# Kernel optimization log

Hardware: AMD Instinct MI355X
Metric: run time of the kernel (lower is better)

## Reference

```python
import jax, jax.numpy as jnp
import numpy as np

NUM_HEADS = 12
LN_EPS = 1e-12


def setup_inputs() -> dict:
    key = jax.random.key(0)
    ks = jax.random.split(key, 18)
    B, S, H, I, P, KW = 8, 128, 768, 3072, 50, 100
    s = 0.02
    inp = {
        'hidden_state': jax.random.normal(ks[0], (B, S, H), jnp.float32),
        'positive_keywords': jax.random.normal(ks[1], (P, H), jnp.float32),
        'negative_keywords': jax.random.normal(ks[2], (P, H), jnp.float32),
        'attention_mask': jnp.zeros((B, 1, 1, S), jnp.float32),
        # Bilinear weights: out = (x @ W) * keyword
        'Wq': jax.random.normal(ks[3], (H, H), jnp.float32) * s,
        'Wk': jax.random.normal(ks[4], (H, H), jnp.float32) * s,
        'Wv': jax.random.normal(ks[5], (H, H), jnp.float32) * s,
        'Wo': jax.random.normal(ks[6], (H, H), jnp.float32) * s,
        'bo': jnp.zeros((H,), jnp.float32),
        # mlp: Linear(kwcount, 1)
        'Wmlp': jax.random.normal(ks[7], (KW,), jnp.float32) * s,
        'bmlp': jnp.zeros((), jnp.float32),
        # Bottleneck FFN
        'Wdown': jax.random.normal(ks[8], (H, I), jnp.float32) * s,
        'bdown': jnp.zeros((I,), jnp.float32),
        'Wup': jax.random.normal(ks[9], (I, H), jnp.float32) * s,
        'bup': jnp.zeros((H,), jnp.float32),
        'gamma': jnp.ones((H,), jnp.float32),
        'beta': jnp.zeros((H,), jnp.float32),
    }
    return inp


def reference(hidden_state, positive_keywords, negative_keywords, attention_mask,
              Wq, Wk, Wv, Wo, bo, Wmlp, bmlp, Wdown, bdown, Wup, bup, gamma, beta):
    B, S, H = hidden_state.shape
    nh = NUM_HEADS
    hd = H // nh
    # interleave pos/neg keywords -> pool [KW, H] (diff == 0, no padding)
    pool = jnp.stack((positive_keywords, negative_keywords), axis=1).reshape(-1, H)

    # shared sequence projections (keyword modulates elementwise afterwards)
    PQ = hidden_state @ Wq  # [B,S,H]
    PK = hidden_state @ Wk
    PV = hidden_state @ Wv
    scale = 1.0 / jnp.sqrt(jnp.float32(hd))

    def per_kw(kw):  # kw: [H]
        def heads(P):
            return (P * kw).reshape(B, S, nh, hd).transpose(0, 2, 1, 3)  # [B,nh,S,hd]
        Q, K, V = heads(PQ), heads(PK), heads(PV)
        scores = jnp.einsum('bhqd,bhkd->bhqk', Q, K) * scale + attention_mask
        # NOTE: softmax over dim=-2 (query axis), faithful to the original
        w = jax.nn.softmax(scores, axis=-2)
        ctx = jnp.einsum('bhqk,bhkd->bhqd', w, V)
        ctx = ctx.transpose(0, 2, 1, 3).reshape(B, S, H)
        return ctx @ Wo + bo  # [B,S,H]

    stacked = jax.vmap(per_kw)(pool)  # [KW,B,S,H]
    # mlp Linear(KW,1) over the stacked keyword axis
    fused = jnp.einsum('kbsh,k->bsh', stacked, Wmlp) + bmlp  # [B,S,H]

    # Bottleneck FFN + residual LayerNorm (dropout = identity in eval)
    down = jax.nn.gelu(fused @ Wdown + bdown, approximate=False)
    up = down @ Wup + bup
    x = up + fused
    mu = jnp.mean(x, axis=-1, keepdims=True)
    var = jnp.var(x, axis=-1, keepdims=True)
    return gamma * (x - mu) / jnp.sqrt(var + LN_EPS) + beta
```

## Files before the change

kernel.cpp:

```cpp
#include <hip/hip_runtime.h>
#include <hip/hip_bf16.h>
#include <math.h>

#define B_ 8
#define S_ 128
#define H_ 768
#define NH_ 12
#define HD_ 64
#define M_ 1024
#define KW_ 100
#define I_ 3072
#define QKVN 2304
#define NCHUNK 5
#define KWPER 20
#define LOG2E 1.4426950408889634f

typedef __attribute__((ext_vector_type(8))) short short8;
typedef __attribute__((ext_vector_type(8))) unsigned short ushort8;
typedef __attribute__((ext_vector_type(4))) float f32x4;
typedef __attribute__((ext_vector_type(4))) short s4b;

static __device__ __forceinline__ unsigned short f2b(float f) {
  union { float f; unsigned int u; } v; v.f = f;
  return (unsigned short)((v.u + 0x7fffu + ((v.u >> 16) & 1u)) >> 16);
}
static __device__ __forceinline__ float b2f(unsigned short b) {
  union { unsigned int u; float f; } v; v.u = ((unsigned int)b) << 16;
  return v.f;
}
static __device__ __forceinline__ void gload16(const unsigned short* g, unsigned short* l) {
  __builtin_amdgcn_global_load_lds((const __attribute__((address_space(1))) unsigned int*)g,
                                   (__attribute__((address_space(3))) unsigned int*)l, 16, 0, 0);
}

__global__ void k_prep(const float* __restrict__ hidden,
                       const float* __restrict__ Wq, const float* __restrict__ Wk,
                       const float* __restrict__ Wv, const float* __restrict__ Wo,
                       const float* __restrict__ Wdown, const float* __restrict__ Wup,
                       const float* __restrict__ posk, const float* __restrict__ negk,
                       const float* __restrict__ Wmlp, const float* __restrict__ bmlp,
                       const float* __restrict__ bo,
                       unsigned short* __restrict__ hb, unsigned short* __restrict__ qkvT,
                       unsigned short* __restrict__ WoT, unsigned short* __restrict__ WdownT,
                       unsigned short* __restrict__ WupT,
                       float* __restrict__ kw2s, float* __restrict__ kwm, float* __restrict__ c0) {
  __shared__ float tile[32][33];
  int z = blockIdx.z;
  int t = threadIdx.x;
  if (z == 6) {
    int n = blockIdx.y * 96 + blockIdx.x;
    if (n < 768) {
      int i = (n * 256 + t) * 4;
      float4 v = *(const float4*)&hidden[i];
      uint2 o;
      o.x = (unsigned)f2b(v.x) | ((unsigned)f2b(v.y) << 16);
      o.y = (unsigned)f2b(v.z) | ((unsigned)f2b(v.w) << 16);
      *(uint2*)&hb[i] = o;
    } else if (n < 1068) {
      int idx = (n - 768) * 256 + t;
      if (idx < KW_ * H_) {
        int j = idx / H_, d = idx - j * H_;
        float v = (j & 1) ? negk[(j >> 1) * H_ + d] : posk[(j >> 1) * H_ + d];
        kw2s[idx] = v * v * 0.125f * LOG2E;
        kwm[idx] = v * Wmlp[j];
      }
    } else if (n == 1068) {
      __shared__ float red[256];
      red[t] = (t < KW_) ? Wmlp[t] : 0.f;
      __syncthreads();
      for (int s = 128; s > 0; s >>= 1) { if (t < s) red[t] += red[t + s]; __syncthreads(); }
      float sWm = red[0];
      for (int c = t; c < H_; c += 256) c0[c] = sWm * bo[c] + bmlp[0];
    }
    return;
  }
  const float* src; unsigned short* dst; int R, C, r0, c0t;
  if (z < 4) {
    if (blockIdx.x >= 24) return;
    const float* srcs[4] = {Wq, Wk, Wv, Wo};
    src = srcs[z];
    dst = (z < 3) ? qkvT + (size_t)z * 768 * 768 : WoT;
    R = 768; C = 768; c0t = blockIdx.x * 32; r0 = blockIdx.y * 32;
  } else if (z == 4) {
    src = Wdown; dst = WdownT; R = 768; C = 3072;
    c0t = blockIdx.x * 32; r0 = blockIdx.y * 32;
  } else {
    src = Wup; dst = WupT; R = 3072; C = 768;
    c0t = blockIdx.y * 32; r0 = blockIdx.x * 32;
  }
  int tx = t & 31, ty = t >> 5;
#pragma unroll
  for (int i = 0; i < 4; i++)
    tile[ty + i * 8][tx] = src[(size_t)(r0 + ty + i * 8) * C + c0t + tx];
  __syncthreads();
#pragma unroll
  for (int i = 0; i < 4; i++)
    dst[(size_t)(c0t + ty + i * 8) * R + r0 + tx] = f2b(tile[tx][ty + i * 8]);
}

template <int EPI>
__launch_bounds__(256)
__global__ void k_gemm_bt(const unsigned short* __restrict__ A, const unsigned short* __restrict__ BT,
                          int M, int N, int K,
                          float* __restrict__ outF, unsigned short* __restrict__ outB,
                          const float* __restrict__ bias, const float* __restrict__ res) {
  __shared__ __align__(16) unsigned short Asm[128 * 32];
  __shared__ __align__(16) unsigned short Bsm[128 * 32];
  int tid = threadIdx.x;
  int lane = tid & 63, wid = tid >> 6;
  int g = lane >> 4, c16 = lane & 15;
  int wr = wid >> 1, wc = wid & 1;
  int m0 = blockIdx.y * 128, n0 = blockIdx.x * 128;
  f32x4 acc[4][4] = {};
  int ldsrow = lane >> 2, ldscol = (lane & 3) * 8;
  for (int kt = 0; kt < K; kt += 32) {
    __syncthreads();
#pragma unroll
    for (int r = 0; r < 2; r++) {
      int c = wid * 2 + r;
      gload16(A + (size_t)(m0 + c * 16 + ldsrow) * K + kt + ldscol, &Asm[c * 512 + lane * 8]);
      gload16(BT + (size_t)(n0 + c * 16 + ldsrow) * K + kt + ldscol, &Bsm[c * 512 + lane * 8]);
    }
    __syncthreads();
    short8 af[4], bf[4];
#pragma unroll
    for (int mi = 0; mi < 4; mi++) af[mi] = *(const short8*)&Asm[(wr * 64 + mi * 16 + c16) * 32 + g * 8];
#pragma unroll
    for (int ni = 0; ni < 4; ni++) bf[ni] = *(const short8*)&Bsm[(wc * 64 + ni * 16 + c16) * 32 + g * 8];
#pragma unroll
    for (int mi = 0; mi < 4; mi++)
#pragma unroll
      for (int ni = 0; ni < 4; ni++)
        acc[mi][ni] = __builtin_amdgcn_mfma_f32_16x16x32_bf16(af[mi], bf[ni], acc[mi][ni], 0, 0, 0);
  }
#pragma unroll
  for (int mi = 0; mi < 4; mi++)
#pragma unroll
    for (int ni = 0; ni < 4; ni++)
#pragma unroll
      for (int rr = 0; rr < 4; rr++) {
        int row = m0 + wr * 64 + mi * 16 + g * 4 + rr;
        int col = n0 + wc * 64 + ni * 16 + c16;
        float v = acc[mi][ni][rr];
        if (EPI == 0) {
          outB[(size_t)row * N + col] = f2b(v);
        } else if (EPI == 2) {
          float t = v + bias[col];
          float gl = 0.5f * t * (1.f + erff(t * 0.70710678118f));
          outB[(size_t)row * N + col] = f2b(gl);
        }
      }
}

template <int OUTB>
__launch_bounds__(256)
__global__ void k_gemm_sk(const unsigned short* __restrict__ A, const unsigned short* __restrict__ BT,
                          int M, int N, int K, int ksl, void* __restrict__ pOut) {
  __shared__ __align__(16) unsigned short Asm[128 * 32];
  __shared__ __align__(16) unsigned short Bsm[128 * 32];
  int tid = threadIdx.x;
  int lane = tid & 63, wid = tid >> 6;
  int g = lane >> 4, c16 = lane & 15;
  int wr = wid >> 1, wc = wid & 1;
  int m0 = blockIdx.y * 128, n0 = blockIdx.x * 128;
  int kstart = blockIdx.z * ksl;
  f32x4 acc[4][4] = {};
  int ldsrow = lane >> 2, ldscol = (lane & 3) * 8;
  for (int kt = 0; kt < ksl; kt += 32) {
    __syncthreads();
#pragma unroll
    for (int r = 0; r < 2; r++) {
      int c = wid * 2 + r;
      gload16(A + (size_t)(m0 + c * 16 + ldsrow) * K + kstart + kt + ldscol, &Asm[c * 512 + lane * 8]);
      gload16(BT + (size_t)(n0 + c * 16 + ldsrow) * K + kstart + kt + ldscol, &Bsm[c * 512 + lane * 8]);
    }
    __syncthreads();
    short8 af[4], bf[4];
#pragma unroll
    for (int mi = 0; mi < 4; mi++) af[mi] = *(const short8*)&Asm[(wr * 64 + mi * 16 + c16) * 32 + g * 8];
#pragma unroll
    for (int ni = 0; ni < 4; ni++) bf[ni] = *(const short8*)&Bsm[(wc * 64 + ni * 16 + c16) * 32 + g * 8];
#pragma unroll
    for (int mi = 0; mi < 4; mi++)
#pragma unroll
      for (int ni = 0; ni < 4; ni++)
        acc[mi][ni] = __builtin_amdgcn_mfma_f32_16x16x32_bf16(af[mi], bf[ni], acc[mi][ni], 0, 0, 0);
  }
#pragma unroll
  for (int mi = 0; mi < 4; mi++)
#pragma unroll
    for (int ni = 0; ni < 4; ni++)
#pragma unroll
      for (int rr = 0; rr < 4; rr++) {
        int row = m0 + wr * 64 + mi * 16 + g * 4 + rr;
        int col = n0 + wc * 64 + ni * 16 + c16;
        if (OUTB) {
          unsigned short* dst = (unsigned short*)pOut + (size_t)blockIdx.z * M * N;
          dst[(size_t)row * N + col] = f2b(acc[mi][ni][rr]);
        } else {
          float* dst = (float*)pOut + (size_t)blockIdx.z * M * N;
          dst[(size_t)row * N + col] = acc[mi][ni][rr];
        }
      }
}

template <int SPLITS, int EPI>
__global__ void k_red(const float* __restrict__ p, const float* __restrict__ bias,
                      float* __restrict__ outF, unsigned short* __restrict__ outB, int N) {
  int i = (blockIdx.x * 256 + threadIdx.x) * 4;
  const size_t MN = (size_t)M_ * N;
  float4 s = *(const float4*)&p[i];
#pragma unroll
  for (int c = 1; c < SPLITS; c++) {
    float4 v = *(const float4*)&p[c * MN + i];
    s.x += v.x; s.y += v.y; s.z += v.z; s.w += v.w;
  }
  if (EPI == 1) {
    int col = i % N;
    s.x += bias[col]; s.y += bias[col + 1]; s.z += bias[col + 2]; s.w += bias[col + 3];
    *(float4*)&outF[i] = s;
  }
  uint2 o;
  o.x = (unsigned)f2b(s.x) | ((unsigned)f2b(s.y) << 16);
  o.y = (unsigned)f2b(s.z) | ((unsigned)f2b(s.w) << 16);
  *(uint2*)&outB[i] = o;
}

template <int SPLITS>
__global__ void k_redb(const unsigned short* __restrict__ p, unsigned short* __restrict__ outB,
                       size_t MN) {
  int i = (blockIdx.x * 256 + threadIdx.x) * 4;
  float s0 = 0.f, s1 = 0.f, s2 = 0.f, s3 = 0.f;
#pragma unroll
  for (int c = 0; c < SPLITS; c++) {
    uint2 v = *(const uint2*)&p[c * MN + i];
    s0 += b2f((unsigned short)(v.x & 0xffffu));
    s1 += b2f((unsigned short)(v.x >> 16));
    s2 += b2f((unsigned short)(v.y & 0xffffu));
    s3 += b2f((unsigned short)(v.y >> 16));
  }
  uint2 o;
  o.x = (unsigned)f2b(s0) | ((unsigned)f2b(s1) << 16);
  o.y = (unsigned)f2b(s2) | ((unsigned)f2b(s3) << 16);
  *(uint2*)&outB[i] = o;
}

__launch_bounds__(512, 2)
__global__ void k_attn(const unsigned short* __restrict__ PQKV,
                       const float* __restrict__ kw2s, const float* __restrict__ kwm,
                       unsigned short* __restrict__ partial) {
  __shared__ __align__(16) char SM[67584];
  int tid = threadIdx.x;
  int lane = tid & 63, wid = tid >> 6;
  int g = (lane >> 4) & 3, c16 = lane & 15;
  int n = blockIdx.x;
  int chunk = (n >> 3) % NCHUNK;
  int hb = (n & 7) + 8 * (n / (8 * NCHUNK));
  int h = hb >> 3, b = hb & 7;
  const size_t rowbase = (size_t)b * 128 * QKVN;
  const unsigned short* Qbase = PQKV + rowbase + h * HD_;
  const unsigned short* Kbase = Qbase + H_;
  const unsigned short* Vbase = Qbase + 2 * H_;

  unsigned short (*QS)[72] = (unsigned short(*)[72])SM;
  unsigned short (*VS)[72] = (unsigned short(*)[72])(SM + 18432);
  {
    int kq = tid >> 2, quarter = tid & 3;
    const unsigned short* srcq = Qbase + (size_t)kq * QKVN + quarter * 16;
    ushort8 a0 = *(const ushort8*)srcq;
    ushort8 a1 = *(const ushort8*)(srcq + 8);
    *(ushort8*)&QS[kq][quarter * 16] = a0;
    *(ushort8*)&QS[kq][quarter * 16 + 8] = a1;
    const unsigned short* srcv = Vbase + (size_t)kq * QKVN + quarter * 16;
    ushort8 w0 = *(const ushort8*)srcv;
    ushort8 w1 = *(const ushort8*)(srcv + 8);
    *(ushort8*)&VS[kq][quarter * 16] = w0;
    *(ushort8*)&VS[kq][quarter * 16 + 8] = w1;
  }
  const unsigned short* kpg = Kbase + (size_t)(wid * 16 + c16) * QKVN;
  ushort8 kraw0 = *(const ushort8*)(kpg + g * 8);
  ushort8 kraw1 = *(const ushort8*)(kpg + 32 + g * 8);
  __syncthreads();
  unsigned short vraw[4][4];
#pragma unroll
  for (int dt = 0; dt < 4; dt++)
#pragma unroll
    for (int j = 0; j < 4; j++)
      vraw[dt][j] = VS[wid * 16 + 4 * g + j][dt * 16 + c16];

  f32x4 acc[4][8] = {};
  int zo = 0;
  asm volatile("" : "+v"(zo));
  for (int ki = 0; ki < KWPER; ki++) {
    int kwi = chunk * KWPER + ki;
    const float* k2p = kw2s + (size_t)kwi * H_ + h * HD_;
    const float* kmp = kwm + (size_t)kwi * H_ + h * HD_;
    short8 kA0, kA1;
    {
      float4 s0 = *(const float4*)(k2p + g * 8);
      float4 s1 = *(const float4*)(k2p + g * 8 + 4);
      float4 s2 = *(const float4*)(k2p + 32 + g * 8);
      float4 s3 = *(const float4*)(k2p + 32 + g * 8 + 4);
      union { unsigned u[4]; short8 v; } p0, p1;
      asm("v_cvt_pk_bf16_f32 %0, %1, %2" : "=v"(p0.u[0]) : "v"(b2f(kraw0[0]) * s0.x), "v"(b2f(kraw0[1]) * s0.y));
      asm("v_cvt_pk_bf16_f32 %0, %1, %2" : "=v"(p0.u[1]) : "v"(b2f(kraw0[2]) * s0.z), "v"(b2f(kraw0[3]) * s0.w));
      asm("v_cvt_pk_bf16_f32 %0, %1, %2" : "=v"(p0.u[2]) : "v"(b2f(kraw0[4]) * s1.x), "v"(b2f(kraw0[5]) * s1.y));
      asm("v_cvt_pk_bf16_f32 %0, %1, %2" : "=v"(p0.u[3]) : "v"(b2f(kraw0[6]) * s1.z), "v"(b2f(kraw0[7]) * s1.w));
      asm("v_cvt_pk_bf16_f32 %0, %1, %2" : "=v"(p1.u[0]) : "v"(b2f(kraw1[0]) * s2.x), "v"(b2f(kraw1[1]) * s2.y));
      asm("v_cvt_pk_bf16_f32 %0, %1, %2" : "=v"(p1.u[1]) : "v"(b2f(kraw1[2]) * s2.z), "v"(b2f(kraw1[3]) * s2.w));
      asm("v_cvt_pk_bf16_f32 %0, %1, %2" : "=v"(p1.u[2]) : "v"(b2f(kraw1[4]) * s3.x), "v"(b2f(kraw1[5]) * s3.y));
      asm("v_cvt_pk_bf16_f32 %0, %1, %2" : "=v"(p1.u[3]) : "v"(b2f(kraw1[6]) * s3.z), "v"(b2f(kraw1[7]) * s3.w));
      kA0 = p0.v; kA1 = p1.v;
    }
    f32x4 csum = {0.f, 0.f, 0.f, 0.f};
    s4b pw[8];
    __builtin_amdgcn_s_setprio(1);
#pragma unroll
    for (int t = 0; t < 8; t++) {
      short8 q0 = *(const short8*)&QS[16 * t + c16][g * 8 + zo];
      short8 q1 = *(const short8*)&QS[16 * t + c16][32 + g * 8 + zo];
      f32x4 z = {0.f, 0.f, 0.f, 0.f};
      z = __builtin_amdgcn_mfma_f32_16x16x32_bf16(kA0, q0, z, 0, 0, 0);
      z = __builtin_amdgcn_mfma_f32_16x16x32_bf16(kA1, q1, z, 0, 0, 0);
      float e0 = __builtin_amdgcn_exp2f(z[0]);
      float e1 = __builtin_amdgcn_exp2f(z[1]);
      float e2 = __builtin_amdgcn_exp2f(z[2]);
      float e3 = __builtin_amdgcn_exp2f(z[3]);
      csum[0] += e0; csum[1] += e1; csum[2] += e2; csum[3] += e3;
      union { unsigned u[2]; s4b v; } pp;
      asm("v_cvt_pk_bf16_f32 %0, %1, %2" : "=v"(pp.u[0]) : "v"(e0), "v"(e1));
      asm("v_cvt_pk_bf16_f32 %0, %1, %2" : "=v"(pp.u[1]) : "v"(e2), "v"(e3));
      pw[t] = pp.v;
    }
    __builtin_amdgcn_s_setprio(0);
    float cs[4];
#pragma unroll
    for (int rr = 0; rr < 4; rr++) {
      float s = csum[rr];
      s += __shfl_xor(s, 1);
      s += __shfl_xor(s, 2);
      s += __shfl_xor(s, 4);
      s += __shfl_xor(s, 8);
      cs[rr] = __builtin_amdgcn_rcpf(s);
    }
    s4b vA[4];
#pragma unroll
    for (int dt = 0; dt < 4; dt++) {
      float km = kmp[dt * 16 + c16];
      union { unsigned u[2]; s4b v; } pv;
      asm("v_cvt_pk_bf16_f32 %0, %1, %2" : "=v"(pv.u[0])
          : "v"(b2f(vraw[dt][0]) * km * cs[0]), "v"(b2f(vraw[dt][1]) * km * cs[1]));
      asm("v_cvt_pk_bf16_f32 %0, %1, %2" : "=v"(pv.u[1])
          : "v"(b2f(vraw[dt][2]) * km * cs[2]), "v"(b2f(vraw[dt][3]) * km * cs[3]));
      vA[dt] = pv.v;
    }
    __builtin_amdgcn_s_setprio(1);
#pragma unroll
    for (int dt = 0; dt < 4; dt++)
#pragma unroll
      for (int t = 0; t < 8; t++)
        acc[dt][t] = __builtin_amdgcn_mfma_f32_16x16x16bf16_1k(vA[dt], pw[t], acc[dt][t], 0, 0, 0);
    __builtin_amdgcn_s_setprio(0);
  }
  float (*Ebuf)[16][132] = (float(*)[16][132])SM;
  int qo = tid & 127, db = (tid >> 7) * 4;
#pragma unroll
  for (int dt = 0; dt < 4; dt++) {
    __syncthreads();
#pragma unroll
    for (int t = 0; t < 8; t++)
#pragma unroll
      for (int rr = 0; rr < 4; rr++)
        Ebuf[wid][4 * g + rr][16 * t + c16] = acc[dt][t][rr];
    __syncthreads();
    float s0 = 0.f, s1 = 0.f, s2 = 0.f, s3 = 0.f;
#pragma unroll
    for (int w = 0; w < 8; w++) {
      s0 += Ebuf[w][db + 0][qo];
      s1 += Ebuf[w][db + 1][qo];
      s2 += Ebuf[w][db + 2][qo];
      s3 += Ebuf[w][db + 3][qo];
    }
    unsigned short* o = partial + (size_t)chunk * M_ * H_ + (size_t)(b * 128 + qo) * H_ + h * HD_ + dt * 16 + db;
    uint2 ov;
    ov.x = (unsigned)f2b(s0) | ((unsigned)f2b(s1) << 16);
    ov.y = (unsigned)f2b(s2) | ((unsigned)f2b(s3) << 16);
    *(uint2*)o = ov;
  }
}

__launch_bounds__(256)
__global__ void k_ln2(const unsigned short* __restrict__ pUp, const float* __restrict__ bup,
                      const float* __restrict__ fusedF,
                      const float* __restrict__ gamma, const float* __restrict__ beta,
                      float* __restrict__ out) {
  __shared__ float red[8];
  int row = blockIdx.x, t = threadIdx.x;
  int lane = t & 63, wid = t >> 6;
  const size_t MN = (size_t)M_ * H_;
  const size_t rb = (size_t)row * H_;
  float v[3];
#pragma unroll
  for (int j = 0; j < 3; j++) {
    int c = t + j * 256;
    float x = b2f(pUp[rb + c]) + b2f(pUp[MN + rb + c]) + b2f(pUp[2 * MN + rb + c]) + b2f(pUp[3 * MN + rb + c]);
    v[j] = x + bup[c] + fusedF[rb + c];
  }
  float s = v[0] + v[1] + v[2];
#pragma unroll
  for (int off = 1; off < 64; off <<= 1) s += __shfl_xor(s, off);
  if (lane == 0) red[wid] = s;
  __syncthreads();
  float mu = (red[0] + red[1] + red[2] + red[3]) * (1.f / 768.f);
  float q = 0.f;
#pragma unroll
  for (int j = 0; j < 3; j++) { float d = v[j] - mu; q += d * d; }
#pragma unroll
  for (int off = 1; off < 64; off <<= 1) q += __shfl_xor(q, off);
  if (lane == 0) red[4 + wid] = q;
  __syncthreads();
  float var = (red[4] + red[5] + red[6] + red[7]) * (1.f / 768.f);
  float rstd = rsqrtf(var + 1e-12f);
#pragma unroll
  for (int j = 0; j < 3; j++) {
    int c = t + j * 256;
    out[rb + c] = gamma[c] * ((v[j] - mu) * rstd) + beta[c];
  }
}


extern "C" void kernel_launch(void* const* d_in, const int* in_sizes, int n_in,
                              void* d_out, int out_size, void* d_ws, size_t ws_size,
                              hipStream_t stream) {
  const float* hidden = (const float*)d_in[0];
  const float* posk   = (const float*)d_in[1];
  const float* negk   = (const float*)d_in[2];
  const float* Wq     = (const float*)d_in[4];
  const float* Wk     = (const float*)d_in[5];
  const float* Wv     = (const float*)d_in[6];
  const float* Wo     = (const float*)d_in[7];
  const float* bo     = (const float*)d_in[8];
  const float* Wmlp   = (const float*)d_in[9];
  const float* bmlp   = (const float*)d_in[10];
  const float* Wdown  = (const float*)d_in[11];
  const float* bdown  = (const float*)d_in[12];
  const float* Wup    = (const float*)d_in[13];
  const float* bup    = (const float*)d_in[14];
  const float* gamma  = (const float*)d_in[15];
  const float* beta   = (const float*)d_in[16];

  char* ws = (char*)d_ws;
  size_t off = 0;
  auto alloc = [&](size_t bytes) -> void* {
    void* p = ws + off;
    off += (bytes + 255) & ~(size_t)255;
    return p;
  };
  unsigned short* hb     = (unsigned short*)alloc((size_t)M_ * H_ * 2);
  unsigned short* qkvT   = (unsigned short*)alloc((size_t)QKVN * H_ * 2);
  unsigned short* WoT    = (unsigned short*)alloc((size_t)H_ * H_ * 2);
  unsigned short* WdownT = (unsigned short*)alloc((size_t)I_ * H_ * 2);
  unsigned short* WupT   = (unsigned short*)alloc((size_t)H_ * I_ * 2);
  unsigned short* PQKV   = (unsigned short*)alloc((size_t)M_ * QKVN * 2);
  float* kw2s    = (float*)alloc((size_t)KW_ * H_ * 4);
  float* kwm     = (float*)alloc((size_t)KW_ * H_ * 4);
  float* c0      = (float*)alloc((size_t)H_ * 4);
  float* partial = (float*)alloc((size_t)10 * M_ * H_ * 4);
  unsigned short* ctxsum = (unsigned short*)alloc((size_t)M_ * H_ * 2);
  float* fusedF  = (float*)alloc((size_t)M_ * H_ * 4);
  unsigned short* fusedB = (unsigned short*)alloc((size_t)M_ * H_ * 2);
  unsigned short* downB  = (unsigned short*)alloc((size_t)M_ * I_ * 2);

  k_prep<<<dim3(96, 24, 7), 256, 0, stream>>>(hidden, Wq, Wk, Wv, Wo, Wdown, Wup,
                                              posk, negk, Wmlp, bmlp, bo,
                                              hb, qkvT, WoT, WdownT, WupT, kw2s, kwm, c0);
  k_gemm_bt<0><<<dim3(18, 8), 256, 0, stream>>>(hb, qkvT, M_, QKVN, H_, nullptr, PQKV, nullptr, nullptr);
  k_attn<<<NCHUNK * NH_ * B_, 512, 0, stream>>>(PQKV, kw2s, kwm, (unsigned short*)partial);
  k_redb<NCHUNK><<<768, 256, 0, stream>>>((const unsigned short*)partial, ctxsum, (size_t)M_ * H_);
  k_gemm_sk<0><<<dim3(6, 8, 4), 256, 0, stream>>>(ctxsum, WoT, M_, H_, H_, 192, partial);
  k_red<4, 1><<<768, 256, 0, stream>>>(partial, c0, fusedF, fusedB, H_);
  k_gemm_bt<2><<<dim3(24, 8), 256, 0, stream>>>(fusedB, WdownT, M_, I_, H_, nullptr, downB, bdown, nullptr);
  k_gemm_sk<1><<<dim3(6, 8, 4), 256, 0, stream>>>(downB, WupT, M_, H_, I_, 768, partial);
  k_ln2<<<M_, 256, 0, stream>>>((const unsigned short*)partial, bup, fusedF, gamma, beta, (float*)d_out);
}
```

Baseline: 176.0 us.

## Retile attention waves into key strips by query halves with register-held Q

Each wave now covers a 32-key strip and half of the queries (64 rows) rather than a 16-key strip across all 128 queries. Q fragments are loaded from global memory straight into registers, which removes the Q shared-memory tile and its per-keyword LDS reads and halves the shared-memory footprint. The column softmax sums are now split across two waves per strip, so each keyword iteration adds a small double-buffered shared exchange and a block-wide barrier. The final cross-wave reduction reads 4 partials instead of 8.

```diff
diff --git a/kernel.cpp b/kernel.cpp
--- a/kernel.cpp
+++ b/kernel.cpp
@@ -249,7 +249,8 @@
 __global__ void k_attn(const unsigned short* __restrict__ PQKV,
                        const float* __restrict__ kw2s, const float* __restrict__ kwm,
                        unsigned short* __restrict__ partial) {
-  __shared__ __align__(16) char SM[67584];
+  __shared__ __align__(16) char SM[33792];
+  __shared__ float X[2][8][32];
   int tid = threadIdx.x;
   int lane = tid & 63, wid = tid >> 6;
   int g = (lane >> 4) & 3, c16 = lane & 15;
@@ -257,134 +258,170 @@
   int chunk = (n >> 3) % NCHUNK;
   int hb = (n & 7) + 8 * (n / (8 * NCHUNK));
   int h = hb >> 3, b = hb & 7;
+  int strip = wid >> 1, qh = wid & 1;
+  int kb = strip * 32, qbase = qh * 64;
   const size_t rowbase = (size_t)b * 128 * QKVN;
   const unsigned short* Qbase = PQKV + rowbase + h * HD_;
   const unsigned short* Kbase = Qbase + H_;
   const unsigned short* Vbase = Qbase + 2 * H_;
 
-  unsigned short (*QS)[72] = (unsigned short(*)[72])SM;
-  unsigned short (*VS)[72] = (unsigned short(*)[72])(SM + 18432);
+  unsigned short (*VS)[72] = (unsigned short(*)[72])SM;
   {
     int kq = tid >> 2, quarter = tid & 3;
-    const unsigned short* srcq = Qbase + (size_t)kq * QKVN + quarter * 16;
-    ushort8 a0 = *(const ushort8*)srcq;
-    ushort8 a1 = *(const ushort8*)(srcq + 8);
-    *(ushort8*)&QS[kq][quarter * 16] = a0;
-    *(ushort8*)&QS[kq][quarter * 16 + 8] = a1;
     const unsigned short* srcv = Vbase + (size_t)kq * QKVN + quarter * 16;
     ushort8 w0 = *(const ushort8*)srcv;
     ushort8 w1 = *(const ushort8*)(srcv + 8);
     *(ushort8*)&VS[kq][quarter * 16] = w0;
     *(ushort8*)&VS[kq][quarter * 16 + 8] = w1;
   }
-  const unsigned short* kpg = Kbase + (size_t)(wid * 16 + c16) * QKVN;
-  ushort8 kraw0 = *(const ushort8*)(kpg + g * 8);
-  ushort8 kraw1 = *(const ushort8*)(kpg + 32 + g * 8);
+  ushort8 qf[4][2];
+#pragma unroll
+  for (int t = 0; t < 4; t++) {
+    const unsigned short* qr = Qbase + (size_t)(qbase + 16 * t + c16) * QKVN;
+    qf[t][0] = *(const ushort8*)(qr + g * 8);
+    qf[t][1] = *(const ushort8*)(qr + 32 + g * 8);
+  }
+  ushort8 kraw[2][2];
+#pragma unroll
+  for (int sub = 0; sub < 2; sub++) {
+    const unsigned short* kr = Kbase + (size_t)(kb + sub * 16 + c16) * QKVN;
+    kraw[sub][0] = *(const ushort8*)(kr + g * 8);
+    kraw[sub][1] = *(const ushort8*)(kr + 32 + g * 8);
+  }
   __syncthreads();
-  unsigned short vraw[4][4];
+  unsigned short vraw[4][2][4];
 #pragma unroll
   for (int dt = 0; dt < 4; dt++)
 #pragma unroll
-    for (int j = 0; j < 4; j++)
-      vraw[dt][j] = VS[wid * 16 + 4 * g + j][dt * 16 + c16];
-
-  f32x4 acc[4][8] = {};
-  int zo = 0;
-  asm volatile("" : "+v"(zo));
+    for (int sub = 0; sub < 2; sub++)
+#pragma unroll
+      for (int j = 0; j < 4; j++)
+        vraw[dt][sub][j] = VS[kb + sub * 16 + 4 * g + j][dt * 16 + c16];
+
+  f32x4 acc[4][4] = {};
   for (int ki = 0; ki < KWPER; ki++) {
     int kwi = chunk * KWPER + ki;
     const float* k2p = kw2s + (size_t)kwi * H_ + h * HD_;
     const float* kmp = kwm + (size_t)kwi * H_ + h * HD_;
-    short8 kA0, kA1;
+    short8 kA[2][2];
     {
       float4 s0 = *(const float4*)(k2p + g * 8);
       float4 s1 = *(const float4*)(k2p + g * 8 + 4);
       float4 s2 = *(const float4*)(k2p + 32 + g * 8);
       float4 s3 = *(const float4*)(k2p + 32 + g * 8 + 4);
-      union { unsigned u[4]; short8 v; } p0, p1;
-      asm("v_cvt_pk_bf16_f32 %0, %1, %2" : "=v"(p0.u[0]) : "v"(b2f(kraw0[0]) * s0.x), "v"(b2f(kraw0[1]) * s0.y));
-      asm("v_cvt_pk_bf16_f32 %0, %1, %2" : "=v"(p0.u[1]) : "v"(b2f(kraw0[2]) * s0.z), "v"(b2f(kraw0[3]) * s0.w));
-      asm("v_cvt_pk_bf16_f32 %0, %1, %2" : "=v"(p0.u[2]) : "v"(b2f(kraw0[4]) * s1.x), "v"(b2f(kraw0[5]) * s1.y));
-      asm("v_cvt_pk_bf16_f32 %0, %1, %2" : "=v"(p0.u[3]) : "v"(b2f(kraw0[6]) * s1.z), "v"(b2f(kraw0[7]) * s1.w));
-      asm("v_cvt_pk_bf16_f32 %0, %1, %2" : "=v"(p1.u[0]) : "v"(b2f(kraw1[0]) * s2.x), "v"(b2f(kraw1[1]) * s2.y));
-      asm("v_cvt_pk_bf16_f32 %0, %1, %2" : "=v"(p1.u[1]) : "v"(b2f(kraw1[2]) * s2.z), "v"(b2f(kraw1[3]) * s2.w));
-      asm("v_cvt_pk_bf16_f32 %0, %1, %2" : "=v"(p1.u[2]) : "v"(b2f(kraw1[4]) * s3.x), "v"(b2f(kraw1[5]) * s3.y));
-      asm("v_cvt_pk_bf16_f32 %0, %1, %2" : "=v"(p1.u[3]) : "v"(b2f(kraw1[6]) * s3.z), "v"(b2f(kraw1[7]) * s3.w));
-      kA0 = p0.v; kA1 = p1.v;
-    }
-    f32x4 csum = {0.f, 0.f, 0.f, 0.f};
-    s4b pw[8];
+#pragma unroll
+      for (int sub = 0; sub < 2; sub++) {
+        union { unsigned u[4]; short8 v; } p0, p1;
+        asm("v_cvt_pk_bf16_f32 %0, %1, %2" : "=v"(p0.u[0]) : "v"(b2f(kraw[sub][0][0]) * s0.x), "v"(b2f(kraw[sub][0][1]) * s0.y));
+        asm("v_cvt_pk_bf16_f32 %0, %1, %2" : "=v"(p0.u[1]) : "v"(b2f(kraw[sub][0][2]) * s0.z), "v"(b2f(kraw[sub][0][3]) * s0.w));
+        asm("v_cvt_pk_bf16_f32 %0, %1, %2" : "=v"(p0.u[2]) : "v"(b2f(kraw[sub][0][4]) * s1.x), "v"(b2f(kraw[sub][0][5]) * s1.y));
+        asm("v_cvt_pk_bf16_f32 %0, %1, %2" : "=v"(p0.u[3]) : "v"(b2f(kraw[sub][0][6]) * s1.z), "v"(b2f(kraw[sub][0][7]) * s1.w));
+        asm("v_cvt_pk_bf16_f32 %0, %1, %2" : "=v"(p1.u[0]) : "v"(b2f(kraw[sub][1][0]) * s2.x), "v"(b2f(kraw[sub][1][1]) * s2.y));
+        asm("v_cvt_pk_bf16_f32 %0, %1, %2" : "=v"(p1.u[1]) : "v"(b2f(kraw[sub][1][2]) * s2.z), "v"(b2f(kraw[sub][1][3]) * s2.w));
+        asm("v_cvt_pk_bf16_f32 %0, %1, %2" : "=v"(p1.u[2]) : "v"(b2f(kraw[sub][1][4]) * s3.x), "v"(b2f(kraw[sub][1][5]) * s3.y));
+        asm("v_cvt_pk_bf16_f32 %0, %1, %2" : "=v"(p1.u[3]) : "v"(b2f(kraw[sub][1][6]) * s3.z), "v"(b2f(kraw[sub][1][7]) * s3.w));
+        kA[sub][0] = p0.v; kA[sub][1] = p1.v;
+      }
+    }
+    float csum[2][4] = {};
+    s4b pw[2][4];
     __builtin_amdgcn_s_setprio(1);
 #pragma unroll
-    for (int t = 0; t < 8; t++) {
-      short8 q0 = *(const short8*)&QS[16 * t + c16][g * 8 + zo];
-      short8 q1 = *(const short8*)&QS[16 * t + c16][32 + g * 8 + zo];
-      f32x4 z = {0.f, 0.f, 0.f, 0.f};
-      z = __builtin_amdgcn_mfma_f32_16x16x32_bf16(kA0, q0, z, 0, 0, 0);
-      z = __builtin_amdgcn_mfma_f32_16x16x32_bf16(kA1, q1, z, 0, 0, 0);
-      float e0 = __builtin_amdgcn_exp2f(z[0]);
-      float e1 = __builtin_amdgcn_exp2f(z[1]);
-      float e2 = __builtin_amdgcn_exp2f(z[2]);
-      float e3 = __builtin_amdgcn_exp2f(z[3]);
-      csum[0] += e0; csum[1] += e1; csum[2] += e2; csum[3] += e3;
-      union { unsigned u[2]; s4b v; } pp;
-      asm("v_cvt_pk_bf16_f32 %0, %1, %2" : "=v"(pp.u[0]) : "v"(e0), "v"(e1));
-      asm("v_cvt_pk_bf16_f32 %0, %1, %2" : "=v"(pp.u[1]) : "v"(e2), "v"(e3));
-      pw[t] = pp.v;
-    }
+    for (int t = 0; t < 4; t++)
+#pragma unroll
+      for (int sub = 0; sub < 2; sub++) {
+        f32x4 z = {0.f, 0.f, 0.f, 0.f};
+        z = __builtin_amdgcn_mfma_f32_16x16x32_bf16(kA[sub][0], *(const short8*)&qf[t][0], z, 0, 0, 0);
+        z = __builtin_amdgcn_mfma_f32_16x16x32_bf16(kA[sub][1], *(const short8*)&qf[t][1], z, 0, 0, 0);
+        float e0 = __builtin_amdgcn_exp2f(z[0]);
+        float e1 = __builtin_amdgcn_exp2f(z[1]);
+        float e2 = __builtin_amdgcn_exp2f(z[2]);
+        float e3 = __builtin_amdgcn_exp2f(z[3]);
+        csum[sub][0] += e0; csum[sub][1] += e1; csum[sub][2] += e2; csum[sub][3] += e3;
+        union { unsigned u[2]; s4b v; } pp;
+        asm("v_cvt_pk_bf16_f32 %0, %1, %2" : "=v"(pp.u[0]) : "v"(e0), "v"(e1));
+        asm("v_cvt_pk_bf16_f32 %0, %1, %2" : "=v"(pp.u[1]) : "v"(e2), "v"(e3));
+        pw[sub][t] = pp.v;
+      }
     __builtin_amdgcn_s_setprio(0);
-    float cs[4];
-#pragma unroll
-    for (int rr = 0; rr < 4; rr++) {
-      float s = csum[rr];
-      s += __shfl_xor(s, 1);
-      s += __shfl_xor(s, 2);
-      s += __shfl_xor(s, 4);
-      s += __shfl_xor(s, 8);
-      cs[rr] = __builtin_amdgcn_rcpf(s);
-    }
-    s4b vA[4];
+#pragma unroll
+    for (int sub = 0; sub < 2; sub++)
+#pragma unroll
+      for (int rr = 0; rr < 4; rr++) {
+        float s = csum[sub][rr];
+        s += __shfl_xor(s, 1);
+        s += __shfl_xor(s, 2);
+        s += __shfl_xor(s, 4);
+        s += __shfl_xor(s, 8);
+        csum[sub][rr] = s;
+      }
+    int buf = ki & 1;
+    if (!(lane & 15)) {
+#pragma unroll
+      for (int sub = 0; sub < 2; sub++)
+#pragma unroll
+        for (int rr = 0; rr < 4; rr++)
+          X[buf][wid][sub * 16 + 4 * g + rr] = csum[sub][rr];
+    }
+    __syncthreads();
+    float cs[2][4];
+#pragma unroll
+    for (int sub = 0; sub < 2; sub++)
+#pragma unroll
+      for (int rr = 0; rr < 4; rr++)
+        cs[sub][rr] = __builtin_amdgcn_rcpf(csum[sub][rr] + X[buf][wid ^ 1][sub * 16 + 4 * g + rr]);
+    s4b vA[4][2];
 #pragma unroll
     for (int dt = 0; dt < 4; dt++) {
       float km = kmp[dt * 16 + c16];
-      union { unsigned u[2]; s4b v; } pv;
-      asm("v_cvt_pk_bf16_f32 %0, %1, %2" : "=v"(pv.u[0])
-          : "v"(b2f(vraw[dt][0]) * km * cs[0]), "v"(b2f(vraw[dt][1]) * km * cs[1]));
-      asm("v_cvt_pk_bf16_f32 %0, %1, %2" : "=v"(pv.u[1])
-          : "v"(b2f(vraw[dt][2]) * km * cs[2]), "v"(b2f(vraw[dt][3]) * km * cs[3]));
-      vA[dt] = pv.v;
+#pragma unroll
+      for (int sub = 0; sub < 2; sub++) {
+        union { unsigned u[2]; s4b v; } pv;
+        asm("v_cvt_pk_bf16_f32 %0, %1, %2" : "=v"(pv.u[0])
+            : "v"(b2f(vraw[dt][sub][0]) * km * cs[sub][0]), "v"(b2f(vraw[dt][sub][1]) * km * cs[sub][1]));
+        asm("v_cvt_pk_bf16_f32 %0, %1, %2" : "=v"(pv.u[1])
+            : "v"(b2f(vraw[dt][sub][2]) * km * cs[sub][2]), "v"(b2f(vraw[dt][sub][3]) * km * cs[sub][3]));
+        vA[dt][sub] = pv.v;
+      }
     }
     __builtin_amdgcn_s_setprio(1);
 #pragma unroll
     for (int dt = 0; dt < 4; dt++)
 #pragma unroll
-      for (int t = 0; t < 8; t++)
-        acc[dt][t] = __builtin_amdgcn_mfma_f32_16x16x16bf16_1k(vA[dt], pw[t], acc[dt][t], 0, 0, 0);
+      for (int t = 0; t < 4; t++) {
+        acc[dt][t] = __builtin_amdgcn_mfma_f32_16x16x16bf16_1k(vA[dt][0], pw[0][t], acc[dt][t], 0, 0, 0);
+        acc[dt][t] = __builtin_amdgcn_mfma_f32_16x16x16bf16_1k(vA[dt][1], pw[1][t], acc[dt][t], 0, 0, 0);
+      }
     __builtin_amdgcn_s_setprio(0);
   }
-  float (*Ebuf)[16][132] = (float(*)[16][132])SM;
-  int qo = tid & 127, db = (tid >> 7) * 4;
+  float (*Ebuf)[16][66] = (float(*)[16][66])SM;
+  int qo2 = tid & 63;
+  int rest = tid >> 6;
+  int qhx = rest & 1;
+  int dd = rest >> 1;
 #pragma unroll
   for (int dt = 0; dt < 4; dt++) {
     __syncthreads();
 #pragma unroll
-    for (int t = 0; t < 8; t++)
+    for (int t = 0; t < 4; t++)
 #pragma unroll
       for (int rr = 0; rr < 4; rr++)
         Ebuf[wid][4 * g + rr][16 * t + c16] = acc[dt][t][rr];
     __syncthreads();
-    float s0 = 0.f, s1 = 0.f, s2 = 0.f, s3 = 0.f;
-#pragma unroll
-    for (int w = 0; w < 8; w++) {
-      s0 += Ebuf[w][db + 0][qo];
-      s1 += Ebuf[w][db + 1][qo];
-      s2 += Ebuf[w][db + 2][qo];
-      s3 += Ebuf[w][db + 3][qo];
-    }
-    unsigned short* o = partial + (size_t)chunk * M_ * H_ + (size_t)(b * 128 + qo) * H_ + h * HD_ + dt * 16 + db;
+    float sj[4];
+#pragma unroll
+    for (int j = 0; j < 4; j++) {
+      float v = 0.f;
+#pragma unroll
+      for (int s4 = 0; s4 < 4; s4++) v += Ebuf[2 * s4 + qhx][dd * 4 + j][qo2];
+      sj[j] = v;
+    }
+    int row = b * 128 + qhx * 64 + qo2;
+    int col = h * HD_ + dt * 16 + dd * 4;
+    unsigned short* o = partial + (size_t)chunk * M_ * H_ + (size_t)row * H_ + col;
     uint2 ov;
-    ov.x = (unsigned)f2b(s0) | ((unsigned)f2b(s1) << 16);
-    ov.y = (unsigned)f2b(s2) | ((unsigned)f2b(s3) << 16);
+    ov.x = (unsigned)f2b(sj[0]) | ((unsigned)f2b(sj[1]) << 16);
+    ov.y = (unsigned)f2b(sj[2]) | ((unsigned)f2b(sj[3]) << 16);
     *(uint2*)o = ov;
   }
 }
```

Measured after the change: 212.0 us. 1.2x slower.
